# Performance work log

Hardware: AMD Instinct MI355X
Metric: run time of the kernel (lower is better)

Reference implementation:

```python
import jax, jax.numpy as jnp
import numpy as np

TEMPERATURE = 0.6
TOP_K = 50
TOP_P = 0.9
REP_PENALTY = 1.2
BATCH, VOCAB, HIST = 256, 128000, 200


def setup_inputs() -> dict:
    key = jax.random.key(0)
    k1, k2 = jax.random.split(key)
    logits = jax.random.normal(k1, (BATCH, VOCAB), dtype=jnp.float32)
    prev_tokens = jax.random.randint(k2, (BATCH, HIST), 0, VOCAB)
    return {"logits": logits, "prev_tokens": prev_tokens}


def reference(logits, prev_tokens):
    B = logits.shape[0]
    rows = jnp.arange(B)[:, None]  # [B,1] row index for scatter

    # --- repetition penalty: mult if <0 else div, on previously seen tokens ---
    vals = jnp.take_along_axis(logits, prev_tokens, axis=1)  # [B,H]
    penalized = jnp.where(vals < 0, vals * REP_PENALTY, vals / REP_PENALTY)
    logits = logits.at[rows, prev_tokens].set(penalized)

    # --- temperature ---
    logits = logits / TEMPERATURE

    # --- top-k filter: mask everything below the k-th largest logit ---
    kth = jax.lax.top_k(logits, TOP_K)[0][:, -1:]  # [B,1]
    logits = jnp.where(logits < kth, -jnp.inf, logits)

    # --- top-p (nucleus) filter: sort desc, cumsum probs, keep prefix <= p ---
    order = jnp.argsort(-logits, axis=-1)                      # [B,V] desc order
    sorted_logits = jnp.take_along_axis(logits, order, axis=-1)
    cum_probs = jnp.cumsum(jax.nn.softmax(sorted_logits, axis=-1), axis=-1)
    remove_sorted = cum_probs > TOP_P
    # shift right so the first token exceeding p is kept (HF semantics)
    remove_sorted = jnp.concatenate(
        [jnp.zeros_like(remove_sorted[:, :1]), remove_sorted[:, :-1]], axis=-1)
    # scatter mask back to vocab order
    remove = jnp.zeros_like(remove_sorted).at[rows, order].set(remove_sorted)
    logits = jnp.where(remove, -jnp.inf, logits)

    # --- distribution parameter of Multinomial(total_count=compare_sample) ---
    probs = jax.nn.softmax(logits, axis=-1)
    return probs
```

## Files before the change

kernel.cpp:

```cpp
#include <hip/hip_runtime.h>
#include <stdint.h>

#define BATCH    256
#define VOCAB    128000
#define HIST     200
#define TOPK     50
#define CAP      2048
#define MINCNT   250
#define T_RAW    2.6f
#define CHUNKS_PER_ROW 8
#define P1_THREADS 256
#define F4T      16
#define CH4      (VOCAB / 4 / CHUNKS_PER_ROW)
#define LOCCAP   768
#define P2_THREADS 512
#define BITWORDS (VOCAB / 32)

typedef unsigned long long ull;

__device__ __forceinline__ unsigned fkey_of(float f) {
  unsigned u = __float_as_uint(f);
  return (u & 0x80000000u) ? ~u : (u | 0x80000000u);
}
__device__ __forceinline__ float f_of_key(unsigned k) {
  unsigned u = (k & 0x80000000u) ? (k & 0x7FFFFFFFu) : ~k;
  return __uint_as_float(u);
}

__global__ __launch_bounds__(P1_THREADS) void phase1_kernel(
    const float* __restrict__ logits,
    int* __restrict__ cnt_g, ull* __restrict__ cand)
{
  __shared__ ull cand_loc[LOCCAP];
  __shared__ int s_n, s_base;
  if (threadIdx.x == 0) s_n = 0;
  __syncthreads();

  const int blk = blockIdx.x;
  const int b   = blk >> 3;
  const int c   = blk & 7;
  const float4* row4 = (const float4*)(logits + (size_t)b * VOCAB) + (size_t)c * CH4;
  const int base_idx = c * CH4 * 4;
  const int t = threadIdx.x;

  float4 vals[F4T];
  #pragma unroll
  for (int u = 0; u < F4T; ++u) {
    int i = t + u * P1_THREADS;
    vals[u] = (i < CH4) ? row4[i]
                        : make_float4(-1e30f, -1e30f, -1e30f, -1e30f);
  }
  float mx = -1e30f;
  #pragma unroll
  for (int u = 0; u < F4T; ++u) {
    float m01 = fmaxf(vals[u].x, vals[u].y);
    float m23 = fmaxf(vals[u].z, vals[u].w);
    mx = fmaxf(mx, fmaxf(m01, m23));
  }
  if (mx > T_RAW) {
    #pragma unroll
    for (int u = 0; u < F4T; ++u) {
      int i = t + u * P1_THREADS;
      float vv[4] = {vals[u].x, vals[u].y, vals[u].z, vals[u].w};
      #pragma unroll
      for (int l = 0; l < 4; ++l) {
        if (vv[l] > T_RAW) {
          int p = atomicAdd(&s_n, 1);
          if (p < LOCCAP)
            cand_loc[p] = ((ull)fkey_of(vv[l]) << 32) |
                          (unsigned)(~(unsigned)(base_idx + i * 4 + l));
        }
      }
    }
  }
  __syncthreads();

  int n = s_n;
  bool overflow = (n > LOCCAP);
  if (overflow) n = LOCCAP;
  if (threadIdx.x == 0)
    s_base = atomicAdd(&cnt_g[b], n + (overflow ? (1 << 20) : 0));
  __syncthreads();
  const int base = s_base;
  for (int i = threadIdx.x; i < n; i += P1_THREADS) {
    int p = base + i;
    if (p < CAP) cand[(size_t)b * CAP + p] = cand_loc[i];
  }
}

__global__ __launch_bounds__(P2_THREADS) void phase2_kernel(
    const float* __restrict__ logits, const int* __restrict__ prev,
    float* __restrict__ out, const int* __restrict__ cnt_g,
    const ull* __restrict__ cand)
{
  __shared__ unsigned bitmask[BITWORDS];
  __shared__ ull keys[CAP];
  __shared__ float evals[CAP];
  __shared__ int s_cnt, s_m, s_j;
  __shared__ float s_Z2;

  const int b = blockIdx.x, tid = threadIdx.x;

  for (int i = tid; i < BITWORDS; i += P2_THREADS) bitmask[i] = 0u;
  __syncthreads();
  for (int i = tid; i < HIST; i += P2_THREADS) {
    int t = prev[b * HIST + i];
    atomicOr(&bitmask[t >> 5], 1u << (t & 31));
  }
  __syncthreads();

  const int cnt_raw = cnt_g[b];
  if (cnt_raw >= MINCNT && cnt_raw <= CAP) {
    for (int i = tid; i < cnt_raw; i += P2_THREADS) {
      ull key = cand[(size_t)b * CAP + i];
      unsigned iv = (unsigned)(key & 0xFFFFFFFFull);
      int idx = (int)(~iv);
      float v = f_of_key((unsigned)(key >> 32));
      float y = v;
      if ((bitmask[idx >> 5] >> (idx & 31)) & 1u)
        y = (v < 0.0f) ? v * 1.2f : v / 1.2f;
      float x = y / 0.6f;
      keys[i] = ((ull)fkey_of(x) << 32) | iv;
    }
    if (tid == 0) s_cnt = cnt_raw;
    __syncthreads();
  } else {
    const float* row = logits + (size_t)b * VOCAB;
    float T = 3.0f, Tlo = 0.f, Thi = 0.f;
    bool hasLo = false, hasHi = false;
    int c2 = 0;
    for (int attempt = 0; attempt < 40; ++attempt) {
      __syncthreads();
      if (tid == 0) s_cnt = 0;
      __syncthreads();
      for (int i = tid; i < VOCAB; i += P2_THREADS) {
        float v = row[i];
        float y = v;
        if ((bitmask[i >> 5] >> (i & 31)) & 1u)
          y = (v < 0.0f) ? v * 1.2f : v / 1.2f;
        if (y > T) {
          int pos = atomicAdd(&s_cnt, 1);
          if (pos < CAP) {
            float x = y / 0.6f;
            keys[pos] = ((ull)fkey_of(x) << 32) | (unsigned)(~(unsigned)i);
          }
        }
      }
      __syncthreads();
      c2 = s_cnt;
      if (c2 >= TOPK && c2 <= CAP) break;
      if (c2 < TOPK) { Thi = T; hasHi = true; T = hasLo ? 0.5f * (T + Tlo) : T - 1.0f; }
      else           { Tlo = T; hasLo = true; T = hasHi ? 0.5f * (T + Thi) : T + 1.0f; }
    }
    __syncthreads();
    if (tid == 0 && s_cnt > CAP) s_cnt = CAP;
    __syncthreads();
  }
  const int m_cnt = s_cnt;

  int n = 64;
  while (n < m_cnt) n <<= 1;
  for (int i = m_cnt + tid; i < n; i += P2_THREADS) keys[i] = 0ull;
  __syncthreads();
  for (int k = 2; k <= n; k <<= 1) {
    for (int j = k >> 1; j > 0; j >>= 1) {
      for (int i = tid; i < n; i += P2_THREADS) {
        int l = i ^ j;
        if (l > i) {
          ull a = keys[i], cc = keys[l];
          bool up = (i & k) == 0;
          if (up ? (a < cc) : (a > cc)) { keys[i] = cc; keys[l] = a; }
        }
      }
      __syncthreads();
    }
  }

  if (tid == 0) {
    int kk = (m_cnt < TOPK) ? m_cnt : TOPK;
    unsigned kth = (unsigned)(keys[kk - 1] >> 32);
    int m = kk;
    while (m < m_cnt && (unsigned)(keys[m] >> 32) == kth) m++;
    s_m = m;
  }
  __syncthreads();
  const int m = s_m;
  const float maxx = f_of_key((unsigned)(keys[0] >> 32));
  for (int i = tid; i < m; i += P2_THREADS)
    evals[i] = expf(f_of_key((unsigned)(keys[i] >> 32)) - maxx);
  __syncthreads();

  if (tid == 0) {
    float Z = 0.f;
    for (int i = 0; i < m; ++i) Z += evals[i];
    float cum = 0.f;
    int j = 0;
    for (int i = 0; i < m; ++i) {
      if (i > 0 && cum > 0.9f) break;
      cum += evals[i] / Z;
      j = i + 1;
    }
    float Z2 = 0.f;
    for (int i = 0; i < j; ++i) Z2 += evals[i];
    s_j = j; s_Z2 = Z2;
  }
  __syncthreads();

  for (int i = tid; i < s_j; i += P2_THREADS) {
    int idx = (int)(~(unsigned)(keys[i] & 0xFFFFFFFFull));
    out[(size_t)b * VOCAB + idx] = evals[i] / s_Z2;
  }
}

__global__ __launch_bounds__(1024) void sample_head_kernel(
    const float* __restrict__ logits, const int* __restrict__ prev,
    float* __restrict__ out)
{
  __shared__ unsigned bitmask[BITWORDS];
  __shared__ ull keys[CAP];
  __shared__ float evals[CAP];
  __shared__ int s_count;
  __shared__ int s_m, s_j;
  __shared__ float s_maxx, s_Z2;

  const int b   = blockIdx.x;
  const int tid = threadIdx.x;
  const float* row  = logits + (size_t)b * VOCAB;
  float*       orow = out    + (size_t)b * VOCAB;

  for (int i = tid; i < BITWORDS; i += 1024) bitmask[i] = 0u;
  __syncthreads();
  for (int i = tid; i < HIST; i += 1024) {
    int t = prev[b * HIST + i];
    atomicOr(&bitmask[t >> 5], 1u << (t & 31));
  }
  __syncthreads();

  float T = 3.0f;
  float Tlo = 0.f, Thi = 0.f;
  bool hasLo = false, hasHi = false;
  int cnt = 0;

  const float4* row4  = (const float4*)row;
  float4*       orow4 = (float4*)orow;
  const int N4 = VOCAB / 4;

  for (int attempt = 0; attempt < 40; ++attempt) {
    __syncthreads();
    if (tid == 0) s_count = 0;
    __syncthreads();
    for (int i = tid; i < N4; i += 1024) {
      float4 v4 = row4[i];
      if (attempt == 0) orow4[i] = make_float4(0.f, 0.f, 0.f, 0.f);
      int v0 = i * 4;
      unsigned w  = bitmask[v0 >> 5];
      unsigned sh = v0 & 31;
      float vv[4] = {v4.x, v4.y, v4.z, v4.w};
      #pragma unroll
      for (int l = 0; l < 4; ++l) {
        float v = vv[l];
        float y = v;
        if ((w >> (sh + l)) & 1u)
          y = (v < 0.0f) ? v * 1.2f : v / 1.2f;
        if (y > T) {
          float x = y / 0.6f;
          int pos = atomicAdd(&s_count, 1);
          if (pos < CAP) {
            keys[pos] = ((ull)fkey_of(x) << 32) | (unsigned)(~(unsigned)(v0 + l));
          }
        }
      }
    }
    __syncthreads();
    cnt = s_count;
    if (cnt >= TOPK && cnt <= CAP) break;
    if (cnt < TOPK) { Thi = T; hasHi = true; T = hasLo ? 0.5f * (T + Tlo) : T - 1.0f; }
    else            { Tlo = T; hasLo = true; T = hasHi ? 0.5f * (T + Thi) : T + 1.0f; }
  }
  if (cnt > CAP) cnt = CAP;

  int n = 64;
  while (n < cnt) n <<= 1;
  for (int i = cnt + tid; i < n; i += 1024) keys[i] = 0ull;
  __syncthreads();
  for (int k = 2; k <= n; k <<= 1) {
    for (int j = k >> 1; j > 0; j >>= 1) {
      for (int i = tid; i < n; i += 1024) {
        int l = i ^ j;
        if (l > i) {
          ull a = keys[i], c = keys[l];
          bool up = (i & k) == 0;
          if (up ? (a < c) : (a > c)) { keys[i] = c; keys[l] = a; }
        }
      }
      __syncthreads();
    }
  }

  if (tid == 0) {
    int kk = (cnt < TOPK) ? cnt : TOPK;
    unsigned kth = (unsigned)(keys[kk - 1] >> 32);
    int m = kk;
    while (m < cnt && (unsigned)(keys[m] >> 32) == kth) m++;
    s_m = m;
    s_maxx = f_of_key((unsigned)(keys[0] >> 32));
  }
  __syncthreads();
  int m = s_m;
  float maxx = s_maxx;
  for (int i = tid; i < m; i += 1024)
    evals[i] = expf(f_of_key((unsigned)(keys[i] >> 32)) - maxx);
  __syncthreads();

  if (tid == 0) {
    float Z = 0.f;
    for (int i = 0; i < m; ++i) Z += evals[i];
    float cum = 0.f;
    int j = 0;
    for (int i = 0; i < m; ++i) {
      if (i > 0 && cum > 0.9f) break;
      cum += evals[i] / Z;
      j = i + 1;
    }
    float Z2 = 0.f;
    for (int i = 0; i < j; ++i) Z2 += evals[i];
    s_j = j; s_Z2 = Z2;
  }
  __syncthreads();

  int j = s_j;
  float Z2 = s_Z2;
  for (int i = tid; i < j; i += 1024) {
    int idx = (int)(~(unsigned)(keys[i] & 0xFFFFFFFFull));
    orow[idx] = evals[i] / Z2;
  }
}

extern "C" void kernel_launch(void* const* d_in, const int* in_sizes, int n_in,
                              void* d_out, int out_size, void* d_ws, size_t ws_size,
                              hipStream_t stream) {
  const float* logits = (const float*)d_in[0];
  const int*   prev   = (const int*)d_in[1];
  float*       out    = (float*)d_out;

  const size_t need = 1024 + (size_t)BATCH * CAP * sizeof(ull);
  if (ws_size >= need) {
    int* cnt = (int*)d_ws;
    ull* cand = (ull*)((char*)d_ws + 1024);
    hipMemsetAsync(d_ws, 0, BATCH * sizeof(int), stream);
    hipMemsetAsync(d_out, 0, (size_t)out_size * sizeof(float), stream);
    hipLaunchKernelGGL(phase1_kernel, dim3(BATCH * CHUNKS_PER_ROW), dim3(P1_THREADS),
                       0, stream, logits, cnt, cand);
    hipLaunchKernelGGL(phase2_kernel, dim3(BATCH), dim3(P2_THREADS),
                       0, stream, logits, prev, out, cnt, cand);
  } else {
    hipLaunchKernelGGL(sample_head_kernel, dim3(BATCH), dim3(1024), 0, stream,
                       logits, prev, out);
  }
}
```

Baseline: 261.2 us.

## Write per-chunk candidate segments instead of global atomic append

Phase 1 now writes each chunk's candidates into its own fixed segment with a per-chunk count, removing the global atomicAdd on a per-row counter and the workspace memset. Phase 2 reads the eight counts, computes prefix offsets and gathers the segments, falling back to the slow full-row path if any segment overflows. The phase 2 block size is doubled to 1024 threads, and the phase 1 load bounds check is limited to the last unrolled iteration. The smaller segment cap makes the fallback path more likely when one chunk has many candidates.

```diff
diff --git a/kernel.cpp b/kernel.cpp
--- a/kernel.cpp
+++ b/kernel.cpp
@@ -9,11 +9,14 @@
 #define MINCNT   250
 #define T_RAW    2.6f
 #define CHUNKS_PER_ROW 8
+#define NCHUNK   (BATCH * CHUNKS_PER_ROW)
+#define CNT_BYTES 16384
 #define P1_THREADS 256
 #define F4T      16
 #define CH4      (VOCAB / 4 / CHUNKS_PER_ROW)
-#define LOCCAP   768
-#define P2_THREADS 512
+#define SEGCAP   256
+#define LOCCAP   512
+#define P2_THREADS 1024
 #define BITWORDS (VOCAB / 32)
 
 typedef unsigned long long ull;
@@ -29,10 +32,10 @@
 
 __global__ __launch_bounds__(P1_THREADS) void phase1_kernel(
     const float* __restrict__ logits,
-    int* __restrict__ cnt_g, ull* __restrict__ cand)
+    int* __restrict__ cnt8, ull* __restrict__ cand)
 {
   __shared__ ull cand_loc[LOCCAP];
-  __shared__ int s_n, s_base;
+  __shared__ int s_n;
   if (threadIdx.x == 0) s_n = 0;
   __syncthreads();
 
@@ -45,10 +48,12 @@
 
   float4 vals[F4T];
   #pragma unroll
-  for (int u = 0; u < F4T; ++u) {
-    int i = t + u * P1_THREADS;
-    vals[u] = (i < CH4) ? row4[i]
-                        : make_float4(-1e30f, -1e30f, -1e30f, -1e30f);
+  for (int u = 0; u < F4T - 1; ++u)
+    vals[u] = row4[t + u * P1_THREADS];
+  {
+    int i = t + (F4T - 1) * P1_THREADS;
+    vals[F4T - 1] = (i < CH4) ? row4[i]
+                              : make_float4(-1e30f, -1e30f, -1e30f, -1e30f);
   }
   float mx = -1e30f;
   #pragma unroll
@@ -64,7 +69,7 @@
       float vv[4] = {vals[u].x, vals[u].y, vals[u].z, vals[u].w};
       #pragma unroll
       for (int l = 0; l < 4; ++l) {
-        if (vv[l] > T_RAW) {
+        if (vv[l] > T_RAW && i < CH4) {
           int p = atomicAdd(&s_n, 1);
           if (p < LOCCAP)
             cand_loc[p] = ((ull)fkey_of(vv[l]) << 32) |
@@ -75,22 +80,16 @@
   }
   __syncthreads();
 
-  int n = s_n;
-  bool overflow = (n > LOCCAP);
-  if (overflow) n = LOCCAP;
-  if (threadIdx.x == 0)
-    s_base = atomicAdd(&cnt_g[b], n + (overflow ? (1 << 20) : 0));
-  __syncthreads();
-  const int base = s_base;
-  for (int i = threadIdx.x; i < n; i += P1_THREADS) {
-    int p = base + i;
-    if (p < CAP) cand[(size_t)b * CAP + p] = cand_loc[i];
-  }
+  const int n = s_n;
+  if (t == 0) cnt8[blk] = n;
+  const int nf = (n < SEGCAP) ? n : SEGCAP;
+  for (int i = t; i < nf; i += P1_THREADS)
+    cand[(size_t)blk * SEGCAP + i] = cand_loc[i];
 }
 
 __global__ __launch_bounds__(P2_THREADS) void phase2_kernel(
     const float* __restrict__ logits, const int* __restrict__ prev,
-    float* __restrict__ out, const int* __restrict__ cnt_g,
+    float* __restrict__ out, const int* __restrict__ cnt8,
     const ull* __restrict__ cand)
 {
   __shared__ unsigned bitmask[BITWORDS];
@@ -109,20 +108,34 @@
   }
   __syncthreads();
 
-  const int cnt_raw = cnt_g[b];
-  if (cnt_raw >= MINCNT && cnt_raw <= CAP) {
-    for (int i = tid; i < cnt_raw; i += P2_THREADS) {
-      ull key = cand[(size_t)b * CAP + i];
-      unsigned iv = (unsigned)(key & 0xFFFFFFFFull);
-      int idx = (int)(~iv);
-      float v = f_of_key((unsigned)(key >> 32));
-      float y = v;
-      if ((bitmask[idx >> 5] >> (idx & 31)) & 1u)
-        y = (v < 0.0f) ? v * 1.2f : v / 1.2f;
-      float x = y / 0.6f;
-      keys[i] = ((ull)fkey_of(x) << 32) | iv;
-    }
-    if (tid == 0) s_cnt = cnt_raw;
+  int n_c[CHUNKS_PER_ROW], off_c[CHUNKS_PER_ROW];
+  int total = 0;
+  bool ok = true;
+  #pragma unroll
+  for (int c = 0; c < CHUNKS_PER_ROW; ++c) {
+    int n = cnt8[b * CHUNKS_PER_ROW + c];
+    n_c[c] = n; off_c[c] = total; total += n;
+    if ((unsigned)n > (unsigned)SEGCAP) ok = false;
+  }
+  if (total < MINCNT || total > CAP) ok = false;
+
+  if (ok) {
+    #pragma unroll
+    for (int c = 0; c < CHUNKS_PER_ROW; ++c) {
+      const ull* seg = cand + (size_t)(b * CHUNKS_PER_ROW + c) * SEGCAP;
+      for (int i = tid; i < n_c[c]; i += P2_THREADS) {
+        ull key = seg[i];
+        unsigned iv = (unsigned)(key & 0xFFFFFFFFull);
+        int idx = (int)(~iv);
+        float v = f_of_key((unsigned)(key >> 32));
+        float y = v;
+        if ((bitmask[idx >> 5] >> (idx & 31)) & 1u)
+          y = (v < 0.0f) ? v * 1.2f : v / 1.2f;
+        float x = y / 0.6f;
+        keys[off_c[c] + i] = ((ull)fkey_of(x) << 32) | iv;
+      }
+    }
+    if (tid == 0) s_cnt = total;
     __syncthreads();
   } else {
     const float* row = logits + (size_t)b * VOCAB;
@@ -343,16 +356,15 @@
   const int*   prev   = (const int*)d_in[1];
   float*       out    = (float*)d_out;
 
-  const size_t need = 1024 + (size_t)BATCH * CAP * sizeof(ull);
+  const size_t need = CNT_BYTES + (size_t)NCHUNK * SEGCAP * sizeof(ull);
   if (ws_size >= need) {
-    int* cnt = (int*)d_ws;
-    ull* cand = (ull*)((char*)d_ws + 1024);
-    hipMemsetAsync(d_ws, 0, BATCH * sizeof(int), stream);
+    int* cnt8 = (int*)d_ws;
+    ull* cand = (ull*)((char*)d_ws + CNT_BYTES);
     hipMemsetAsync(d_out, 0, (size_t)out_size * sizeof(float), stream);
-    hipLaunchKernelGGL(phase1_kernel, dim3(BATCH * CHUNKS_PER_ROW), dim3(P1_THREADS),
-                       0, stream, logits, cnt, cand);
+    hipLaunchKernelGGL(phase1_kernel, dim3(NCHUNK), dim3(P1_THREADS),
+                       0, stream, logits, cnt8, cand);
     hipLaunchKernelGGL(phase2_kernel, dim3(BATCH), dim3(P2_THREADS),
-                       0, stream, logits, prev, out, cnt, cand);
+                       0, stream, logits, prev, out, cnt8, cand);
   } else {
     hipLaunchKernelGGL(sample_head_kernel, dim3(BATCH), dim3(1024), 0, stream,
                        logits, prev, out);
```

New measurement: 255.8 us. -2.1%, faster.
